# Performance work log

Measured on AMD Instinct MI355X. Metric: run time of the kernel, lower is better.

The kernel has to match this reference:

```python
import jax, jax.numpy as jnp
import numpy as np
import math

D = 512
CELLS = 6

def _layer_norm(x, eps=1e-5):
    mu = jnp.mean(x, axis=-1, keepdims=True)
    var = jnp.var(x, axis=-1, keepdims=True)
    return (x - mu) * jax.lax.rsqrt(var + eps)

def setup_inputs() -> dict:
    key = jax.random.key(0)
    k1, k2, k3 = jax.random.split(key, 3)
    B, T = 8, 1024
    x = jax.random.normal(k1, (B * CELLS, T, D), dtype=jnp.float32)
    # causal mask: True = masked (strict upper triangle so diagonal stays valid)
    m = jnp.triu(jnp.ones((T, T), dtype=bool), k=1)
    inhibit = jax.random.normal(k2, (CELLS, CELLS), dtype=jnp.float32) * 0.01
    phases = jnp.linspace(0.0, 2.0 * math.pi, CELLS, dtype=jnp.float32)
    ambition = jnp.ones((CELLS, 1), dtype=jnp.float32) * 0.1
    gate = jax.random.normal(k3, (D, D), dtype=jnp.float32) * 0.02
    return {"x": x, "m": m, "gate": gate, "inhibit": inhibit,
            "phases": phases, "ambition": ambition, "B": B, "T": T}

def reference(x, m, gate, inhibit, phases, ambition, B, T):
    d = gate.shape[0]
    C = inhibit.shape[0]
    nx = _layer_norm(x)
    qkv = nx @ gate                                   # (BC, T, d)
    att = jnp.einsum('btd,bsd->bts', qkv, qkv) * (d ** -0.5)
    att = jnp.where(m, -jnp.inf, att)                 # mask broadcasts over batch
    x = x + jax.nn.softmax(att, axis=-1) @ qkv
    sync = x.reshape(B, C, T, d)
    competed = jnp.einsum('bctd,ck->bktd', sync, inhibit)
    x = x + jnp.tanh(competed).reshape(B * C, T, d)
    p = phases.reshape(1, C, 1, 1)
    a = ambition.reshape(1, C, 1, 1)
    pulse = jnp.sin(x.reshape(B, C, T, d) * a + p)
    return x + pulse.reshape(B * C, T, d) * 0.02
```

## Files before the change

kernel.cpp:

```cpp
#include <hip/hip_runtime.h>
#include <math.h>

typedef __attribute__((ext_vector_type(4))) float f32x4;
typedef __attribute__((ext_vector_type(16))) float f32x16;
typedef __attribute__((ext_vector_type(8))) short s16x8;
typedef __attribute__((ext_vector_type(4))) short s16x4;

#define DD 512
#define TT 1024
#define NB 48

__device__ __forceinline__ short f2bf(float f) {
    union { float f; unsigned u; } v; v.f = f;
    unsigned r = v.u + 0x7fffu + ((v.u >> 16) & 1u);
    return (short)(r >> 16);
}

__device__ __forceinline__ void gll16(const void* g, void* l) {
    __builtin_amdgcn_global_load_lds(
        (const __attribute__((address_space(1))) unsigned int*)g,
        (__attribute__((address_space(3))) unsigned int*)l, 16, 0, 0);
}

__device__ __forceinline__ unsigned pk_bf16(float lo, float hi) {
    unsigned r;
    asm("v_cvt_pk_bf16_f32 %0, %1, %2" : "=v"(r) : "v"(lo), "v"(hi));
    return r;
}

__global__ __launch_bounds__(256) void k_ln_stats(const float* __restrict__ x,
                                                  float* __restrict__ stats) {
    int row = blockIdx.x * 4 + (threadIdx.x >> 6);
    int lane = threadIdx.x & 63;
    const float* p = x + (size_t)row * DD + lane * 8;
    f32x4 a = *(const f32x4*)p;
    f32x4 b = *(const f32x4*)(p + 4);
    float s  = a[0]+a[1]+a[2]+a[3]+b[0]+b[1]+b[2]+b[3];
    float ss = a[0]*a[0]+a[1]*a[1]+a[2]*a[2]+a[3]*a[3]
             + b[0]*b[0]+b[1]*b[1]+b[2]*b[2]+b[3]*b[3];
    #pragma unroll
    for (int off = 32; off >= 1; off >>= 1) {
        s  += __shfl_xor(s, off);
        ss += __shfl_xor(ss, off);
    }
    if (lane == 0) {
        float mu  = s * (1.0f/DD);
        float var = ss * (1.0f/DD) - mu*mu;
        float2 st; st.x = mu; st.y = rsqrtf(var + 1e-5f);
        *(float2*)(stats + (size_t)row*2) = st;
    }
}

__global__ __launch_bounds__(256) void k_gate_t(const float* __restrict__ gate,
                                                short* __restrict__ gateT) {
    __shared__ float tile[64][65];
    int k0 = (blockIdx.x >> 3) * 64;
    int n0 = (blockIdx.x & 7) * 64;
    int tid = threadIdx.x;
    #pragma unroll
    for (int i = 0; i < 16; ++i) {
        int f = i*256 + tid;
        int r = f >> 6, c = f & 63;
        tile[r][c] = gate[(size_t)(k0+r)*DD + n0 + c];
    }
    __syncthreads();
    #pragma unroll
    for (int i = 0; i < 16; ++i) {
        int f = i*256 + tid;
        int r = f >> 6, c = f & 63;
        gateT[(size_t)(n0+r)*DD + k0 + c] = f2bf(tile[c][r]);
    }
}

__global__ __launch_bounds__(256,2) void k_qkv(const float* __restrict__ x,
                                               const float* __restrict__ stats,
                                               const short* __restrict__ gateT,
                                               short* __restrict__ qkv,
                                               short* __restrict__ qkvT) {
    __shared__ __align__(16) short As[128][72];
    __shared__ __align__(16) short Bs[128][72];
    int m0 = (blockIdx.x >> 2) * 128;
    int n0 = (blockIdx.x & 3) * 128;
    int tid = threadIdx.x, lane = tid & 63, w = tid >> 6;
    int wr = w >> 1, wc = w & 1;
    int l15 = lane & 15, lg = lane >> 4;
    f32x4 acc[4][4];
    #pragma unroll
    for (int i=0;i<4;i++)
      #pragma unroll
      for (int j=0;j<4;j++)
        acc[i][j] = (f32x4){0.f,0.f,0.f,0.f};
    for (int kt = 0; kt < 8; ++kt) {
        #pragma unroll
        for (int i = 0; i < 8; ++i) {
            int f4 = i*256 + tid;
            int r  = f4 >> 4;
            int kp = (f4 & 15) * 4;
            f32x4 v = *(const f32x4*)(x + (size_t)(m0+r)*DD + kt*64 + kp);
            float2 st = *(const float2*)(stats + (size_t)(m0+r)*2);
            s16x4 h;
            h[0] = f2bf((v[0]-st.x)*st.y);
            h[1] = f2bf((v[1]-st.x)*st.y);
            h[2] = f2bf((v[2]-st.x)*st.y);
            h[3] = f2bf((v[3]-st.x)*st.y);
            *(s16x4*)(&As[r][kp]) = h;
        }
        #pragma unroll
        for (int i = 0; i < 4; ++i) {
            int f8 = i*256 + tid;
            int r  = f8 >> 3;
            int kp = (f8 & 7) * 8;
            *(s16x8*)(&Bs[r][kp]) = *(const s16x8*)(gateT + (size_t)(n0+r)*DD + kt*64 + kp);
        }
        __syncthreads();
        #pragma unroll
        for (int kk = 0; kk < 2; ++kk) {
            s16x8 af[4], bfr[4];
            #pragma unroll
            for (int mi=0;mi<4;mi++)
                af[mi] = *(const s16x8*)(&As[wr*64 + mi*16 + l15][kk*32 + lg*8]);
            #pragma unroll
            for (int ni=0;ni<4;ni++)
                bfr[ni] = *(const s16x8*)(&Bs[wc*64 + ni*16 + l15][kk*32 + lg*8]);
            #pragma unroll
            for (int mi=0;mi<4;mi++)
              #pragma unroll
              for (int ni=0;ni<4;ni++)
                acc[mi][ni] = __builtin_amdgcn_mfma_f32_16x16x32_bf16(af[mi], bfr[ni], acc[mi][ni], 0,0,0);
        }
        __syncthreads();
    }
    #pragma unroll
    for (int mi=0;mi<4;mi++)
      #pragma unroll
      for (int ni=0;ni<4;ni++) {
        int row0 = m0 + wr*64 + mi*16 + lg*4;
        int col  = n0 + wc*64 + ni*16 + l15;
        s16x4 h4;
        #pragma unroll
        for (int r=0;r<4;r++) h4[r] = f2bf(acc[mi][ni][r]);
        #pragma unroll
        for (int r=0;r<4;r++) qkv[(size_t)(row0+r)*DD + col] = h4[r];
        int b2 = row0 >> 10, t0 = row0 & 1023;
        *(s16x4*)(qkvT + (size_t)b2*DD*TT + (size_t)(t0>>5)*16384
                       + (size_t)col*32 + (t0&31)) = h4;
      }
}

__global__ __launch_bounds__(512,2) void k_attn(const short* __restrict__ qkv,
                                                const short* __restrict__ qkvT,
                                                const float* __restrict__ xin,
                                                float* __restrict__ out) {
    __shared__ __align__(16) short Kt[2][16384];
    __shared__ __align__(16) short Vt[2][16384];
    __shared__ __align__(16) float Sx[8][1024];
    const float scale = 0.044194173824159216f;
    int bid = blockIdx.x;
    int batch = bid % NB;
    int qg = 7 - (bid / NB);
    int tid = threadIdx.x, lane = tid & 63, w = tid >> 6;
    int s = w & 3, dh = w >> 2;
    int l31 = lane & 31, lh = lane >> 5;
    int qb = qg*128 + s*32;
    int qglob = qb + l31;
    const short* gq  = qkv  + (size_t)batch*TT*DD;
    const short* gvt = qkvT + (size_t)batch*DD*TT;

    s16x8 qf[16];
    {
        const short* qrow = gq + (size_t)qglob*DD + dh*256 + lh*8;
        #pragma unroll
        for (int kc=0;kc<16;kc++) qf[kc] = *(const s16x8*)(qrow + kc*16);
    }
    f32x16 o[8];
    #pragma unroll
    for (int m=0;m<8;m++)
        #pragma unroll
        for (int r=0;r<16;r++) o[m][r] = 0.f;
    float m_run = -1e30f, l_run = 0.f;
    int ntile = 4*(qg+1);

    auto stage = [&](int j, int c) {
        const char* ksrc = (const char*)(gq + (size_t)(j*32)*DD);
        char* kdst = (char*)&Kt[c][0];
        #pragma unroll
        for (int i=0;i<4;i++){
            int o16 = i*8192 + w*1024;
            int ol  = o16 + (lane<<4);
            int go  = ol ^ (((ol>>10)&31)<<4);
            gll16(ksrc + go, kdst + o16);
        }
        const char* vsrc = (const char*)(gvt + (size_t)j*16384);
        char* vdst = (char*)&Vt[c][0];
        #pragma unroll
        for (int i=0;i<4;i++){
            int o16 = i*8192 + w*1024;
            int ol  = o16 + (lane<<4);
            int go  = ol ^ (((ol>>7)&3)<<4);
            gll16(vsrc + go, vdst + o16);
        }
    };

    stage(0, 0);
    __syncthreads();
    for (int kj = 0; kj < ntile; ++kj) {
        int cur = kj & 1;
        int kv0 = kj*32;
        if (kj + 1 < ntile) stage(kj+1, (kj+1)&1);
        const char* kbase = (const char*)&Kt[cur][0];
        const char* vbase = (const char*)&Vt[cur][0];
        f32x16 sT;
        #pragma unroll
        for (int r=0;r<16;r++) sT[r] = 0.f;
        #pragma unroll
        for (int kc=0;kc<16;kc++) {
            int boff = (dh*512 + kc*32 + lh*16) ^ (l31 << 4);
            s16x8 kf = *(const s16x8*)(kbase + l31*1024 + boff);
            sT = __builtin_amdgcn_mfma_f32_32x32x16_bf16(kf, qf[kc], sT, 0,0,0);
        }
        {
            float* sw = &Sx[w][0];
            #pragma unroll
            for (int c=0;c<4;c++){
                f32x4 ch = (f32x4){sT[4*c],sT[4*c+1],sT[4*c+2],sT[4*c+3]};
                *(f32x4*)(sw + c*256 + lane*4) = ch;
            }
        }
        asm volatile("s_waitcnt lgkmcnt(0)\n\ts_barrier" ::: "memory");
        float p[16]; float mx = -1e30f;
        {
            const float* sr = &Sx[w^4][0];
            #pragma unroll
            for (int c=0;c<4;c++){
                f32x4 pc = *(const f32x4*)(sr + c*256 + lane*4);
                #pragma unroll
                for (int j=0;j<4;j++){
                    int r = 4*c + j;
                    float v = (sT[r] + pc[j]) * scale;
                    int kvr = kv0 + j + 8*c + 4*lh;
                    if (kvr > qglob) v = -1e30f;
                    p[r] = v;
                    mx = fmaxf(mx, v);
                }
            }
        }
        mx = fmaxf(mx, __shfl_xor(mx, 32));
        if (__any(mx > m_run + 8.0f)) {
            float mn = fmaxf(m_run, mx);
            float alpha = __expf(m_run - mn);
            m_run = mn;
            l_run *= alpha;
            #pragma unroll
            for (int m=0;m<8;m++)
                #pragma unroll
                for (int r=0;r<16;r++) o[m][r] *= alpha;
        }
        float ls = 0.f;
        #pragma unroll
        for (int r=0;r<16;r++){ p[r] = __expf(p[r] - m_run); ls += p[r]; }
        ls += __shfl_xor(ls, 32);
        l_run += ls;
        s16x8 pb[2];
        #pragma unroll
        for (int km=0;km<2;km++){
            int b = 8*km;
            unsigned X0 = pk_bf16(p[b+0], p[b+1]);
            unsigned X1 = pk_bf16(p[b+2], p[b+3]);
            unsigned Y0 = pk_bf16(p[b+4], p[b+5]);
            unsigned Y1 = pk_bf16(p[b+6], p[b+7]);
            asm volatile("v_permlane32_swap_b32 %0, %1" : "+v"(X0), "+v"(Y0));
            asm volatile("v_permlane32_swap_b32 %0, %1" : "+v"(X1), "+v"(Y1));
            union { unsigned u[4]; s16x8 v; } pu;
            pu.u[0] = X0; pu.u[1] = X1; pu.u[2] = Y0; pu.u[3] = Y1;
            pb[km] = pu.v;
        }
        __builtin_amdgcn_s_setprio(1);
        #pragma unroll
        for (int m=0;m<8;m++){
            int row = dh*256 + m*32 + l31;
            #pragma unroll
            for (int km=0;km<2;km++){
                int boff = ((km*32 + lh*16) ^ (((row>>1)&3)<<4));
                s16x8 vf = *(const s16x8*)(vbase + (row<<6) + boff);
                o[m] = __builtin_amdgcn_mfma_f32_32x32x16_bf16(vf, pb[km], o[m], 0,0,0);
            }
        }
        __builtin_amdgcn_s_setprio(0);
        __syncthreads();
    }
    float inv = 1.0f / l_run;
    #pragma unroll
    for (int m=0;m<8;m++)
        #pragma unroll
        for (int r=0;r<16;r++) o[m][r] *= inv;
    float* T = (float*)&Kt[0][0] + w*1152;
    #pragma unroll
    for (int m=0;m<8;m++){
        #pragma unroll
        for (int r=0;r<16;r++){
            int dloc = (r&3) + 8*(r>>2) + 4*lh;
            T[l31*36 + dloc] = o[m][r];
        }
        __builtin_amdgcn_s_waitcnt(0);
        #pragma unroll
        for (int p2=0;p2<4;p2++){
            int qr = p2*8 + (lane>>3);
            f32x4 t = *(const f32x4*)(T + qr*36 + (lane&7)*4);
            size_t gofs = ((size_t)batch*TT + qb + qr)*DD + dh*256 + m*32 + (lane&7)*4;
            f32x4 xi = *(const f32x4*)(xin + gofs);
            *(f32x4*)(out + gofs) = t + xi;
        }
        __builtin_amdgcn_s_waitcnt(0);
    }
}

__device__ __forceinline__ float tanh_fast(float x) {
    float e = __expf(2.0f*x);
    return 1.0f - __fdividef(2.0f, e + 1.0f);
}

__global__ __launch_bounds__(256) void k_post(float* __restrict__ xo,
                                              const float* __restrict__ inhibit,
                                              const float* __restrict__ phases,
                                              const float* __restrict__ ambition) {
    int idx = blockIdx.x*256 + threadIdx.x;
    int b = idx >> 17;
    int rem = idx & 131071;
    size_t base = (size_t)b*6*TT*DD + (size_t)(rem >> 7)*DD + (size_t)(rem & 127)*4;
    f32x4 v[6];
    #pragma unroll
    for (int c=0;c<6;c++) v[c] = *(const f32x4*)(xo + base + (size_t)c*TT*DD);
    float inh[36];
    #pragma unroll
    for (int i=0;i<36;i++) inh[i] = inhibit[i];
    #pragma unroll
    for (int k=0;k<6;k++){
        float c0=0.f, c1=0.f, c2=0.f, c3=0.f;
        #pragma unroll
        for (int c=0;c<6;c++){
            float wv = inh[c*6+k];
            c0 += v[c][0]*wv; c1 += v[c][1]*wv;
            c2 += v[c][2]*wv; c3 += v[c][3]*wv;
        }
        float a = ambition[k], ph = phases[k];
        float x0 = v[k][0] + tanh_fast(c0);
        float x1 = v[k][1] + tanh_fast(c1);
        float x2 = v[k][2] + tanh_fast(c2);
        float x3 = v[k][3] + tanh_fast(c3);
        f32x4 ov;
        ov[0] = x0 + __sinf(x0*a + ph)*0.02f;
        ov[1] = x1 + __sinf(x1*a + ph)*0.02f;
        ov[2] = x2 + __sinf(x2*a + ph)*0.02f;
        ov[3] = x3 + __sinf(x3*a + ph)*0.02f;
        *(f32x4*)(xo + base + (size_t)k*TT*DD) = ov;
    }
}

extern "C" void kernel_launch(void* const* d_in, const int* in_sizes, int n_in,
                              void* d_out, int out_size, void* d_ws, size_t ws_size,
                              hipStream_t stream) {
    (void)in_sizes; (void)n_in; (void)out_size; (void)ws_size;
    const float* x        = (const float*)d_in[0];
    const float* gate     = (const float*)d_in[2];
    const float* inhibit  = (const float*)d_in[3];
    const float* phases   = (const float*)d_in[4];
    const float* ambition = (const float*)d_in[5];
    float* out = (float*)d_out;
    char* ws = (char*)d_ws;
    short* qkv   = (short*)(ws);
    short* qkvT  = (short*)(ws + 50331648);
    float* stats = (float*)(ws + 100663296);
    short* gateT = (short*)(ws + 101056512);

    k_ln_stats <<<dim3(12288), dim3(256), 0, stream>>>(x, stats);
    k_gate_t   <<<dim3(64),    dim3(256), 0, stream>>>(gate, gateT);
    k_qkv      <<<dim3(1536),  dim3(256), 0, stream>>>(x, stats, gateT, qkv, qkvT);
    k_attn     <<<dim3(384),   dim3(512), 0, stream>>>(qkv, qkvT, x, out);
    k_post     <<<dim3(4096),  dim3(256), 0, stream>>>(out, inhibit, phases, ambition);
}
```

Before: 269.0 us.

## Swizzle gateT layout for direct-to-LDS loads and split QK accumulator chains

The gate transpose kernel now writes gateT with an XOR swizzle on 16-byte chunks within each 64-wide k tile. The QKV GEMM then loads its B tile straight into unpadded LDS through global_load_lds and reads it back with the matching swizzle. This drops the register round-trip and the padding while keeping LDS reads free of bank conflicts. Separately, the attention QK^T MFMA chain is split into two independent accumulators that are summed afterwards, which shortens the dependency chain at the cost of extra registers and adds.

```diff
diff --git a/kernel.cpp b/kernel.cpp
--- a/kernel.cpp
+++ b/kernel.cpp
@@ -68,7 +68,9 @@
     for (int i = 0; i < 16; ++i) {
         int f = i*256 + tid;
         int r = f >> 6, c = f & 63;
-        gateT[(size_t)(n0+r)*DD + k0 + c] = f2bf(tile[c][r]);
+        int n = n0 + r, k = k0 + c;
+        int kt = k >> 6, j = (k >> 3) & 7, sub = k & 7;
+        gateT[(size_t)n*DD + kt*64 + ((j ^ (n & 7)) << 3) + sub] = f2bf(tile[c][r]);
     }
 }
 
@@ -78,7 +80,7 @@
                                                short* __restrict__ qkv,
                                                short* __restrict__ qkvT) {
     __shared__ __align__(16) short As[128][72];
-    __shared__ __align__(16) short Bs[128][72];
+    __shared__ __align__(16) short Bs[128][64];
     int m0 = (blockIdx.x >> 2) * 128;
     int n0 = (blockIdx.x & 3) * 128;
     int tid = threadIdx.x, lane = tid & 63, w = tid >> 6;
@@ -91,6 +93,16 @@
       for (int j=0;j<4;j++)
         acc[i][j] = (f32x4){0.f,0.f,0.f,0.f};
     for (int kt = 0; kt < 8; ++kt) {
+        {
+            const char* bsrc = (const char*)gateT + (size_t)n0*1024 + kt*128;
+            char* bdst = (char*)&Bs[0][0];
+            #pragma unroll
+            for (int i=0;i<4;i++){
+                int o16 = (w*4 + i)*1024;
+                int flat = o16 + (lane<<4);
+                gll16(bsrc + (size_t)(flat >> 7)*1024 + (flat & 127), bdst + o16);
+            }
+        }
         #pragma unroll
         for (int i = 0; i < 8; ++i) {
             int f4 = i*256 + tid;
@@ -105,13 +117,6 @@
             h[3] = f2bf((v[3]-st.x)*st.y);
             *(s16x4*)(&As[r][kp]) = h;
         }
-        #pragma unroll
-        for (int i = 0; i < 4; ++i) {
-            int f8 = i*256 + tid;
-            int r  = f8 >> 3;
-            int kp = (f8 & 7) * 8;
-            *(s16x8*)(&Bs[r][kp]) = *(const s16x8*)(gateT + (size_t)(n0+r)*DD + kt*64 + kp);
-        }
         __syncthreads();
         #pragma unroll
         for (int kk = 0; kk < 2; ++kk) {
@@ -120,8 +125,11 @@
             for (int mi=0;mi<4;mi++)
                 af[mi] = *(const s16x8*)(&As[wr*64 + mi*16 + l15][kk*32 + lg*8]);
             #pragma unroll
-            for (int ni=0;ni<4;ni++)
-                bfr[ni] = *(const s16x8*)(&Bs[wc*64 + ni*16 + l15][kk*32 + lg*8]);
+            for (int ni=0;ni<4;ni++){
+                int r = wc*64 + ni*16 + l15;
+                int slot = (kk*4 + lg) ^ (r & 7);
+                bfr[ni] = *(const s16x8*)((const char*)&Bs[0][0] + r*128 + slot*16);
+            }
             #pragma unroll
             for (int mi=0;mi<4;mi++)
               #pragma unroll
@@ -209,20 +217,24 @@
         if (kj + 1 < ntile) stage(kj+1, (kj+1)&1);
         const char* kbase = (const char*)&Kt[cur][0];
         const char* vbase = (const char*)&Vt[cur][0];
-        f32x16 sT;
-        #pragma unroll
-        for (int r=0;r<16;r++) sT[r] = 0.f;
-        #pragma unroll
-        for (int kc=0;kc<16;kc++) {
-            int boff = (dh*512 + kc*32 + lh*16) ^ (l31 << 4);
-            s16x8 kf = *(const s16x8*)(kbase + l31*1024 + boff);
-            sT = __builtin_amdgcn_mfma_f32_32x32x16_bf16(kf, qf[kc], sT, 0,0,0);
+        f32x16 sA, sB;
+        #pragma unroll
+        for (int r=0;r<16;r++){ sA[r]=0.f; sB[r]=0.f; }
+        #pragma unroll
+        for (int kc=0;kc<8;kc++) {
+            int b0 = (dh*512 + (2*kc)*32   + lh*16) ^ (l31 << 4);
+            int b1 = (dh*512 + (2*kc+1)*32 + lh*16) ^ (l31 << 4);
+            s16x8 kf0 = *(const s16x8*)(kbase + l31*1024 + b0);
+            s16x8 kf1 = *(const s16x8*)(kbase + l31*1024 + b1);
+            sA = __builtin_amdgcn_mfma_f32_32x32x16_bf16(kf0, qf[2*kc],   sA, 0,0,0);
+            sB = __builtin_amdgcn_mfma_f32_32x32x16_bf16(kf1, qf[2*kc+1], sB, 0,0,0);
         }
         {
             float* sw = &Sx[w][0];
             #pragma unroll
             for (int c=0;c<4;c++){
-                f32x4 ch = (f32x4){sT[4*c],sT[4*c+1],sT[4*c+2],sT[4*c+3]};
+                f32x4 ch = (f32x4){sA[4*c]+sB[4*c],     sA[4*c+1]+sB[4*c+1],
+                                   sA[4*c+2]+sB[4*c+2], sA[4*c+3]+sB[4*c+3]};
                 *(f32x4*)(sw + c*256 + lane*4) = ch;
             }
         }
@@ -236,7 +248,7 @@
                 #pragma unroll
                 for (int j=0;j<4;j++){
                     int r = 4*c + j;
-                    float v = (sT[r] + pc[j]) * scale;
+                    float v = (sA[r] + sB[r] + pc[j]) * scale;
                     int kvr = kv0 + j + 8*c + 4*lh;
                     if (kvr > qglob) v = -1e30f;
                     p[r] = v;
```

New measurement: 336.5 us. +25.1%, slower.
